# Optimization experiments

Hardware: AMD Instinct MI355X
Metric: run time of the kernel (lower is better)

The kernel has to match this reference:

```python
import jax, jax.numpy as jnp
import numpy as np

EMBED_DIM = 1024
ATTN_DIM = 1024


def setup_inputs() -> dict:
    key = jax.random.key(0)
    k1, k2, k3, k4 = jax.random.split(key, 4)
    scale = 1.0 / np.sqrt(EMBED_DIM)
    return {
        "embedded": jax.random.normal(k1, (4, 2048, EMBED_DIM), dtype=jnp.float32),
        # weights stored as [in, out] (torch Linear applies x @ W.T)
        "Wk": jax.random.uniform(k2, (EMBED_DIM, ATTN_DIM), dtype=jnp.float32, minval=-scale, maxval=scale),
        "Wq": jax.random.uniform(k3, (EMBED_DIM, ATTN_DIM), dtype=jnp.float32, minval=-scale, maxval=scale),
        "Wv": jax.random.uniform(k4, (EMBED_DIM, ATTN_DIM), dtype=jnp.float32, minval=-scale, maxval=scale),
    }


def reference(embedded, Wk, Wq, Wv):
    b, t, _ = embedded.shape
    k = embedded @ Wk  # [b, t, d]
    q = embedded @ Wq
    v = embedded @ Wv
    scores = jnp.einsum("btd,bsd->bts", q, k) / jnp.sqrt(jnp.float32(k.shape[-1]))
    causal = jnp.tril(jnp.ones((t, t), dtype=bool))  # [t, t]
    scores = jnp.where(causal, scores, -jnp.inf)
    w = jax.nn.softmax(scores, axis=-1)
    o = jnp.einsum("bts,bsd->btd", w, v)
    return jnp.round(o * 10000.0) / 10000.0
```

## Files before the change

kernel.cpp:

```cpp
#include <hip/hip_runtime.h>
#include <cmath>

typedef _Float16 half8 __attribute__((ext_vector_type(8)));
typedef _Float16 half4 __attribute__((ext_vector_type(4)));
typedef float floatx4 __attribute__((ext_vector_type(4)));

__device__ __forceinline__ void load_lds16(const void* g, void* l) {
  __builtin_amdgcn_global_load_lds((const __attribute__((address_space(1))) void*)g,
                                   (__attribute__((address_space(3))) void*)l, 16, 0, 0);
}


__global__ void prep_kernel(const float* __restrict__ emb, const float* __restrict__ Wq,
                            const float* __restrict__ Wk, const float* __restrict__ Wv,
                            _Float16* __restrict__ Xp, _Float16* __restrict__ Wqp,
                            _Float16* __restrict__ Wkp, _Float16* __restrict__ Wvtp) {
  int p = blockIdx.x;
  if (p < 640) {
    __shared__ _Float16 lds[16 * 1032];
    const float* src;
    _Float16* dst;
    if (p < 512)      { src = emb + (size_t)p * 16384;        dst = Xp  + (size_t)p * 16384; }
    else if (p < 576) { src = Wq + (size_t)(p - 512) * 16384; dst = Wqp + (size_t)(p - 512) * 16384; }
    else              { src = Wk + (size_t)(p - 576) * 16384; dst = Wkp + (size_t)(p - 576) * 16384; }
    for (int it = 0; it < 16; ++it) {
      int idx = it * 256 + threadIdx.x;
      int row = idx >> 8, c4 = idx & 255;
      float4 v = ((const float4*)src)[row * 256 + c4];
      half4 h;
      h[0] = (_Float16)v.x; h[1] = (_Float16)v.y; h[2] = (_Float16)v.z; h[3] = (_Float16)v.w;
      *(half4*)(lds + row * 1032 + c4 * 4) = h;
    }
    __syncthreads();
    for (int it = 0; it < 8; ++it) {
      int c = it * 256 + threadIdx.x;
      int kb = c >> 6, k16 = (c >> 4) & 3, r = c & 15;
      half8 h = *(const half8*)(lds + r * 1032 + kb * 32 + k16 * 8);
      *(half8*)(dst + (size_t)c * 8) = h;
    }
  } else {
    __shared__ float tile[32][33];
    int q = p - 640;
    int n0 = (q & 31) * 32, k0 = (q >> 5) * 32;
    int c = threadIdx.x & 31, r8 = threadIdx.x >> 5;
    for (int pp = 0; pp < 4; ++pp) {
      int r = pp * 8 + r8;
      tile[r][c] = Wv[(size_t)(k0 + r) * 1024 + n0 + c];
    }
    __syncthreads();
    if (threadIdx.x < 128) {
      int rr = threadIdx.x & 31;
      int k16 = (threadIdx.x >> 5) & 3;
      half8 h;
      for (int kk = 0; kk < 8; ++kk) h[kk] = (_Float16)tile[k16 * 8 + kk][rr];
      int n_row = n0 + rr;
      size_t chunk = ((size_t)(n_row >> 4) * 32 + (k0 >> 5)) * 64 + (k16 << 4) + (n_row & 15);
      *(half8*)(Wvtp + chunk * 8) = h;
    }
  }
}

__device__ __forceinline__ void gemm_core(const _Float16* __restrict__ Ap, int kbA, int tA0,
                                          const _Float16* __restrict__ Bp, int kbB, int tB0,
                                          int kIters, _Float16* sA, _Float16* sB,
                                          floatx4 acc[4][4]) {
  int tid = threadIdx.x;
  int lane = tid & 63, wave = tid >> 6;
  int wm = (wave >> 1) << 6, wn = (wave & 1) << 6;
  const _Float16* gA0 = Ap + ((size_t)(tA0 + 2 * wave) * kbA) * 512 + lane * 8;
  const _Float16* gA1 = Ap + ((size_t)(tA0 + 2 * wave + 1) * kbA) * 512 + lane * 8;
  const _Float16* gB0 = Bp + ((size_t)(tB0 + 2 * wave) * kbB) * 512 + lane * 8;
  const _Float16* gB1 = Bp + ((size_t)(tB0 + 2 * wave + 1) * kbB) * 512 + lane * 8;
  _Float16* lA0 = sA + wave * 1024;
  _Float16* lA1 = lA0 + 512;
  _Float16* lB0 = sB + wave * 1024;
  _Float16* lB1 = lB0 + 512;
  int ta = wm >> 4, tb = wn >> 4, lo = lane * 8;

  for (int kt = 0; kt < kIters; ++kt) {
    size_t kb = (size_t)kt * 512;
    __syncthreads();
    load_lds16(gA0 + kb, lA0);
    load_lds16(gA1 + kb, lA1);
    load_lds16(gB0 + kb, lB0);
    load_lds16(gB1 + kb, lB1);
    __syncthreads();
    half8 af[4], bf[4];
    for (int i = 0; i < 4; ++i) af[i] = *(const half8*)(sA + (ta + i) * 512 + lo);
    for (int j = 0; j < 4; ++j) bf[j] = *(const half8*)(sB + (tb + j) * 512 + lo);
    for (int i = 0; i < 4; ++i)
      for (int j = 0; j < 4; ++j)
        acc[i][j] = __builtin_amdgcn_mfma_f32_16x16x32_f16(af[i], bf[j], acc[i][j], 0, 0, 0);
  }
}

__global__ void mt_kernel(const _Float16* __restrict__ Wkp, const _Float16* __restrict__ Wqp,
                          _Float16* __restrict__ Mtp) {
  __shared__ __align__(16) _Float16 sA[4096];
  __shared__ __align__(16) _Float16 sB[4096];
  floatx4 acc[4][4];
  for (int i = 0; i < 4; ++i)
    for (int j = 0; j < 4; ++j) acc[i][j] = (floatx4){0.f, 0.f, 0.f, 0.f};
  int m0 = blockIdx.y * 128, n0 = blockIdx.x * 128;
  gemm_core(Wkp, 32, m0 >> 4, Wqp, 32, n0 >> 4, 32, sA, sB, acc);
  int lane = threadIdx.x & 63, wave = threadIdx.x >> 6;
  int wm = (wave >> 1) << 6, wn = (wave & 1) << 6;
  int quad = lane >> 4, cl = lane & 15;
  for (int i = 0; i < 4; ++i)
    for (int j = 0; j < 4; ++j)
      for (int rr = 0; rr < 4; ++rr) {
        int row = m0 + wm + i * 16 + quad * 4 + rr;
        int col = n0 + wn + j * 16 + cl;
        size_t chunk = ((size_t)(row >> 4) * 32 + (col >> 5)) * 64 + (((col >> 3) & 3) << 4) + (row & 15);
        Mtp[chunk * 8 + (col & 7)] = (_Float16)acc[i][j][rr];
      }
}

__global__ void proj_kernel(const _Float16* __restrict__ Xp, const _Float16* __restrict__ Bp,
                            _Float16* __restrict__ XMp, _Float16* __restrict__ Vtp) {
  __shared__ __align__(16) _Float16 sA[4096];
  __shared__ __align__(16) _Float16 sB[4096];
  floatx4 acc[4][4];
  for (int i = 0; i < 4; ++i)
    for (int j = 0; j < 4; ++j) acc[i][j] = (floatx4){0.f, 0.f, 0.f, 0.f};
  int m0 = blockIdx.y * 128, n0 = blockIdx.x * 128;
  gemm_core(Xp, 32, m0 >> 4, Bp, 32, n0 >> 4, 32, sA, sB, acc);
  int lane = threadIdx.x & 63, wave = threadIdx.x >> 6;
  int wm = (wave >> 1) << 6, wn = (wave & 1) << 6;
  int quad = lane >> 4, cl = lane & 15;
  int which = n0 >> 10;
  int colbase = (n0 & 1023) + wn;
  for (int i = 0; i < 4; ++i)
    for (int j = 0; j < 4; ++j)
      for (int rr = 0; rr < 4; ++rr) {
        int row_g = m0 + wm + i * 16 + quad * 4 + rr;
        int col = colbase + j * 16 + cl;
        _Float16 val = (_Float16)acc[i][j][rr];
        int b = row_g >> 11, t = row_g & 2047;
        if (which == 1) {
          size_t chunk = ((size_t)(col >> 4) * 64 + (t >> 5)) * 64 + (((t >> 3) & 3) << 4) + (col & 15);
          Vtp[(size_t)b * 2097152 + chunk * 8 + (t & 7)] = val;
        } else {
          size_t chunk = ((size_t)(t >> 4) * 32 + (col >> 5)) * 64 + (((col >> 3) & 3) << 4) + (t & 15);
          XMp[(size_t)b * 2097152 + chunk * 8 + (col & 7)] = val;
        }
      }
}

__global__ void qke_kernel(const _Float16* __restrict__ XMp, const _Float16* __restrict__ Xp,
                           _Float16* __restrict__ E, float* __restrict__ lsum) {
  __shared__ __align__(16) _Float16 sA[4096];
  __shared__ __align__(16) _Float16 sB[4096];
  int x = blockIdx.x, b = blockIdx.y;
  int p = (x & 7) * 17 + (x >> 3);
  int ti = 0;
  while ((ti + 1) * (ti + 2) / 2 <= p) ++ti;
  int tj = p - ti * (ti + 1) / 2;
  const _Float16* Ab = XMp + (size_t)b * 2097152;
  const _Float16* Bb = Xp + (size_t)b * 2097152;
  _Float16* Eb = E + (size_t)b * 4194304;
  floatx4 acc[4][4];
  for (int i = 0; i < 4; ++i)
    for (int j = 0; j < 4; ++j) acc[i][j] = (floatx4){0.f, 0.f, 0.f, 0.f};
  gemm_core(Ab, 32, ti * 8, Bb, 32, tj * 8, 32, sA, sB, acc);
  int lane = threadIdx.x & 63, wave = threadIdx.x >> 6;
  int wm = (wave >> 1) << 6, wn = (wave & 1) << 6;
  int quad = lane >> 4, cl = lane & 15;
  float rs[4][4];
  for (int i = 0; i < 4; ++i)
    for (int rr = 0; rr < 4; ++rr) rs[i][rr] = 0.f;
  for (int i = 0; i < 4; ++i)
    for (int j = 0; j < 4; ++j)
      for (int rr = 0; rr < 4; ++rr) {
        int row = ti * 128 + wm + i * 16 + quad * 4 + rr;
        int col = tj * 128 + wn + j * 16 + cl;
        float e = 0.f;
        if (col <= row) e = __expf(acc[i][j][rr] * 0.03125f - 12.0f);
        _Float16 eh = (_Float16)e;
        rs[i][rr] += (float)eh;
        size_t chunk = ((size_t)(row >> 4) * 64 + (col >> 5)) * 64 + (((col >> 3) & 3) << 4) + (row & 15);
        Eb[chunk * 8 + (col & 7)] = eh;
      }
  float* lb = lsum + (size_t)b * 2048;
  for (int i = 0; i < 4; ++i)
    for (int rr = 0; rr < 4; ++rr) {
      float v = rs[i][rr];
      v += __shfl_xor(v, 1, 64);
      v += __shfl_xor(v, 2, 64);
      v += __shfl_xor(v, 4, 64);
      v += __shfl_xor(v, 8, 64);
      if (cl == 0) atomicAdd(lb + ti * 128 + wm + i * 16 + quad * 4 + rr, v);
    }
}

__global__ void pv_kernel(const _Float16* __restrict__ E, const _Float16* __restrict__ Vtp,
                          const float* __restrict__ lsum, float* __restrict__ out) {
  __shared__ __align__(16) _Float16 sA[4096];
  __shared__ __align__(16) _Float16 sB[4096];
  int n0 = blockIdx.x * 128, b = blockIdx.z;
  int y = blockIdx.y;
  int ti = (y & 1) ? (15 - (y >> 1)) : (y >> 1);
  const _Float16* Pb = E + (size_t)b * 4194304;
  const _Float16* Vb = Vtp + (size_t)b * 2097152;
  floatx4 acc[4][4];
  for (int i = 0; i < 4; ++i)
    for (int j = 0; j < 4; ++j) acc[i][j] = (floatx4){0.f, 0.f, 0.f, 0.f};
  gemm_core(Pb, 64, ti * 8, Vb, 64, n0 >> 4, (ti + 1) * 4, sA, sB, acc);
  int lane = threadIdx.x & 63, wave = threadIdx.x >> 6;
  int wm = (wave >> 1) << 6, wn = (wave & 1) << 6;
  int quad = lane >> 4, cl = lane & 15;
  const float* lb = lsum + (size_t)b * 2048;
  for (int i = 0; i < 4; ++i)
    for (int rr = 0; rr < 4; ++rr) {
      int row = ti * 128 + wm + i * 16 + quad * 4 + rr;
      float inv = 1.0f / lb[row];
      for (int j = 0; j < 4; ++j) {
        int col = n0 + wn + j * 16 + cl;
        float v = acc[i][j][rr] * inv;
        out[((size_t)b * 2048 + row) * 1024 + col] = rintf(v * 10000.f) * 1e-4f;
      }
    }
}

extern "C" void kernel_launch(void* const* d_in, const int* in_sizes, int n_in,
                              void* d_out, int out_size, void* d_ws, size_t ws_size,
                              hipStream_t stream) {
  const float* emb = (const float*)d_in[0];
  const float* Wk = (const float*)d_in[1];
  const float* Wq = (const float*)d_in[2];
  const float* Wv = (const float*)d_in[3];
  float* out = (float*)d_out;

  _Float16* ws = (_Float16*)d_ws;
  _Float16* Xp   = ws;
  _Float16* Wqp  = Xp + (size_t)8192 * 1024;
  _Float16* Wkp  = Wqp + (size_t)1024 * 1024;
  _Float16* Mtp  = Wkp + (size_t)1024 * 1024;
  _Float16* Wvtp = Mtp + (size_t)1024 * 1024;
  _Float16* XMp  = Wvtp + (size_t)1024 * 1024;
  _Float16* Vtp  = XMp + (size_t)8192 * 1024;
  _Float16* Ebuf = Vtp + (size_t)8192 * 1024;
  float* lsum    = (float*)(Ebuf + (size_t)16 * 1024 * 1024);

  hipMemsetAsync(lsum, 0, 4 * 2048 * sizeof(float), stream);
  prep_kernel<<<1664, 256, 0, stream>>>(emb, Wq, Wk, Wv, Xp, Wqp, Wkp, Wvtp);
  mt_kernel<<<dim3(8, 8), 256, 0, stream>>>(Wkp, Wqp, Mtp);
  proj_kernel<<<dim3(16, 64), 256, 0, stream>>>(Xp, Mtp, XMp, Vtp);
  qke_kernel<<<dim3(136, 4), 256, 0, stream>>>(XMp, Xp, Ebuf, lsum);
  pv_kernel<<<dim3(8, 16, 4), 256, 0, stream>>>(Ebuf, Vtp, lsum, out);
}
```

Baseline: 243.7 us.

## Double-buffer LDS in GEMM core and remap block indices for XCD locality

The shared GEMM core now double-buffers its LDS tiles, issuing the direct global-to-LDS loads for the next k-step before computing on the current one. This removes one barrier per iteration and overlaps memory latency with MFMA work, and it raises MFMA wave priority around the compute. The projection and PV kernels also remap block IDs so that consecutive tiles land on the same XCD, aiming for better L2 reuse. LDS use per block doubles, which may lower occupancy.

```diff
diff --git a/kernel.cpp b/kernel.cpp
--- a/kernel.cpp
+++ b/kernel.cpp
@@ -71,33 +71,46 @@
   const _Float16* gA1 = Ap + ((size_t)(tA0 + 2 * wave + 1) * kbA) * 512 + lane * 8;
   const _Float16* gB0 = Bp + ((size_t)(tB0 + 2 * wave) * kbB) * 512 + lane * 8;
   const _Float16* gB1 = Bp + ((size_t)(tB0 + 2 * wave + 1) * kbB) * 512 + lane * 8;
-  _Float16* lA0 = sA + wave * 1024;
-  _Float16* lA1 = lA0 + 512;
-  _Float16* lB0 = sB + wave * 1024;
-  _Float16* lB1 = lB0 + 512;
   int ta = wm >> 4, tb = wn >> 4, lo = lane * 8;
-
+  int wo = wave * 1024;
+
+  load_lds16(gA0, sA + wo);
+  load_lds16(gA1, sA + wo + 512);
+  load_lds16(gB0, sB + wo);
+  load_lds16(gB1, sB + wo + 512);
+  __syncthreads();
+
+  int cur = 0;
   for (int kt = 0; kt < kIters; ++kt) {
-    size_t kb = (size_t)kt * 512;
-    __syncthreads();
-    load_lds16(gA0 + kb, lA0);
-    load_lds16(gA1 + kb, lA1);
-    load_lds16(gB0 + kb, lB0);
-    load_lds16(gB1 + kb, lB1);
-    __syncthreads();
+    if (kt + 1 < kIters) {
+      size_t kb = (size_t)(kt + 1) * 512;
+      int nx = (cur ^ 1) << 12;
+      load_lds16(gA0 + kb, sA + nx + wo);
+      load_lds16(gA1 + kb, sA + nx + wo + 512);
+      load_lds16(gB0 + kb, sB + nx + wo);
+      load_lds16(gB1 + kb, sB + nx + wo + 512);
+    }
+    const _Float16* cA = sA + (cur << 12);
+    const _Float16* cB = sB + (cur << 12);
     half8 af[4], bf[4];
-    for (int i = 0; i < 4; ++i) af[i] = *(const half8*)(sA + (ta + i) * 512 + lo);
-    for (int j = 0; j < 4; ++j) bf[j] = *(const half8*)(sB + (tb + j) * 512 + lo);
+    for (int i = 0; i < 4; ++i) af[i] = *(const half8*)(cA + (ta + i) * 512 + lo);
+    for (int j = 0; j < 4; ++j) bf[j] = *(const half8*)(cB + (tb + j) * 512 + lo);
+    __builtin_amdgcn_s_setprio(1);
     for (int i = 0; i < 4; ++i)
       for (int j = 0; j < 4; ++j)
         acc[i][j] = __builtin_amdgcn_mfma_f32_16x16x32_f16(af[i], bf[j], acc[i][j], 0, 0, 0);
+    __builtin_amdgcn_s_setprio(0);
+    if (kt + 1 < kIters) {
+      __syncthreads();
+      cur ^= 1;
+    }
   }
 }
 
 __global__ void mt_kernel(const _Float16* __restrict__ Wkp, const _Float16* __restrict__ Wqp,
                           _Float16* __restrict__ Mtp) {
-  __shared__ __align__(16) _Float16 sA[4096];
-  __shared__ __align__(16) _Float16 sB[4096];
+  __shared__ __align__(16) _Float16 sA[8192];
+  __shared__ __align__(16) _Float16 sB[8192];
   floatx4 acc[4][4];
   for (int i = 0; i < 4; ++i)
     for (int j = 0; j < 4; ++j) acc[i][j] = (floatx4){0.f, 0.f, 0.f, 0.f};
@@ -118,12 +131,14 @@
 
 __global__ void proj_kernel(const _Float16* __restrict__ Xp, const _Float16* __restrict__ Bp,
                             _Float16* __restrict__ XMp, _Float16* __restrict__ Vtp) {
-  __shared__ __align__(16) _Float16 sA[4096];
-  __shared__ __align__(16) _Float16 sB[4096];
-  floatx4 acc[4][4];
-  for (int i = 0; i < 4; ++i)
-    for (int j = 0; j < 4; ++j) acc[i][j] = (floatx4){0.f, 0.f, 0.f, 0.f};
-  int m0 = blockIdx.y * 128, n0 = blockIdx.x * 128;
+  __shared__ __align__(16) _Float16 sA[8192];
+  __shared__ __align__(16) _Float16 sB[8192];
+  floatx4 acc[4][4];
+  for (int i = 0; i < 4; ++i)
+    for (int j = 0; j < 4; ++j) acc[i][j] = (floatx4){0.f, 0.f, 0.f, 0.f};
+  int orig = blockIdx.y * 16 + blockIdx.x;
+  int tile = (orig & 7) * 128 + (orig >> 3);
+  int m0 = (tile >> 4) * 128, n0 = (tile & 15) * 128;
   gemm_core(Xp, 32, m0 >> 4, Bp, 32, n0 >> 4, 32, sA, sB, acc);
   int lane = threadIdx.x & 63, wave = threadIdx.x >> 6;
   int wm = (wave >> 1) << 6, wn = (wave & 1) << 6;
@@ -149,8 +164,8 @@
 
 __global__ void qke_kernel(const _Float16* __restrict__ XMp, const _Float16* __restrict__ Xp,
                            _Float16* __restrict__ E, float* __restrict__ lsum) {
-  __shared__ __align__(16) _Float16 sA[4096];
-  __shared__ __align__(16) _Float16 sB[4096];
+  __shared__ __align__(16) _Float16 sA[8192];
+  __shared__ __align__(16) _Float16 sB[8192];
   int x = blockIdx.x, b = blockIdx.y;
   int p = (x & 7) * 17 + (x >> 3);
   int ti = 0;
@@ -195,10 +210,13 @@
 
 __global__ void pv_kernel(const _Float16* __restrict__ E, const _Float16* __restrict__ Vtp,
                           const float* __restrict__ lsum, float* __restrict__ out) {
-  __shared__ __align__(16) _Float16 sA[4096];
-  __shared__ __align__(16) _Float16 sB[4096];
-  int n0 = blockIdx.x * 128, b = blockIdx.z;
-  int y = blockIdx.y;
+  __shared__ __align__(16) _Float16 sA[8192];
+  __shared__ __align__(16) _Float16 sB[8192];
+  int orig = blockIdx.x + 8 * (blockIdx.y + 16 * blockIdx.z);
+  int logical = (orig & 7) * 64 + (orig >> 3);
+  int n0 = (logical & 7) * 128;
+  int rest = logical >> 3;
+  int y = rest & 15, b = rest >> 4;
   int ti = (y & 1) ? (15 - (y >> 1)) : (y >> 1);
   const _Float16* Pb = E + (size_t)b * 4194304;
   const _Float16* Vb = Vtp + (size_t)b * 2097152;
```

Measured after the change: 235.0 us. -3.6%, faster.
